# Kernel optimization log

Hardware: AMD Instinct MI355X
Metric: run time of the kernel (lower is better)

## Reference

```python
import jax, jax.numpy as jnp
import numpy as np

N = 50000          # nodes
E = 800000         # edges (avg degree 16)
FEATS = [96, 96, 96, 48]


def setup_inputs() -> dict:
    key = jax.random.key(0)
    ks = jax.random.split(key, 10)
    x = jax.random.normal(ks[0], (N, FEATS[0]), dtype=jnp.float32)
    edge_index = jax.random.randint(ks[1], (2, E), 0, N, dtype=jnp.int64)
    d = {"x": x, "edge_index": edge_index}
    i = 2
    for l in range(3):
        s = 1.0 / np.sqrt(FEATS[l])
        d[f"Wl{l}"] = jax.random.uniform(ks[i], (FEATS[l], FEATS[l + 1]), jnp.float32, -s, s); i += 1
        d[f"Wr{l}"] = jax.random.uniform(ks[i], (FEATS[l], FEATS[l + 1]), jnp.float32, -s, s); i += 1
        d[f"b{l}"] = jnp.zeros((FEATS[l + 1],), jnp.float32)
    return d


def _sage_layer(h, src, dst, Wl, Wr, b, n):
    # PyG SAGEConv (aggr='mean', root_weight=True, normalize=False):
    # out_i = W_l @ mean_{j in N(i)} h_j + W_r @ h_i + b
    msg = h[src]                                                   # [E, F] gather
    ssum = jax.ops.segment_sum(msg, dst, num_segments=n)           # [N, F] scatter-add
    cnt = jax.ops.segment_sum(jnp.ones((src.shape[0], 1), h.dtype), dst, num_segments=n)
    mean = ssum / jnp.maximum(cnt, 1.0)
    return mean @ Wl + h @ Wr + b


def reference(x, edge_index, Wl0, Wr0, b0, Wl1, Wr1, b1, Wl2, Wr2, b2):
    src, dst = edge_index[0], edge_index[1]
    n = x.shape[0]
    # block = SAGEConv -> ReLU -> dropout(identity in eval)
    h = jax.nn.relu(_sage_layer(x, src, dst, Wl0, Wr0, b0, n))
    h = jax.nn.relu(_sage_layer(h, src, dst, Wl1, Wr1, b1, n))
    h = jax.nn.relu(_sage_layer(h, src, dst, Wl2, Wr2, b2, n))
    return h
```

## Files before the change

### kernel.cpp

```cpp
#include <hip/hip_runtime.h>


#define NNODES 50000
#define NROWS  50001
#define ZROW   50000
#define NEDGES 800000
#define CAP    64
#define LSTR   72
#define NBKT   512
#define BKSZ   98
#define NBKB   511
#define EBA    400
#define EPBA   2000
#define SEGC   20
#define CVT_N8 600000
#define CB 2344
#define WTN 46080
#define WB 180

typedef __attribute__((ext_vector_type(8))) short bf16x8;
typedef __attribute__((ext_vector_type(4))) float f32x4;

__device__ inline unsigned short f2bf(float f) {
    unsigned int u = __float_as_uint(f);
    unsigned int r = (u + 0x7fffu + ((u >> 16) & 1u)) >> 16;
    return (unsigned short)r;
}
__device__ inline float bf2f_lo(unsigned int u) { return __uint_as_float(u << 16); }
__device__ inline float bf2f_hi(unsigned int u) { return __uint_as_float(u & 0xffff0000u); }

__global__ void build_a(const int* __restrict__ src, const int* __restrict__ dst,
                        unsigned int* __restrict__ region, unsigned char* __restrict__ cnta,
                        const float* __restrict__ x, unsigned short* __restrict__ h0b,
                        const float* __restrict__ Wl0, const float* __restrict__ Wr0,
                        const float* __restrict__ Wl1, const float* __restrict__ Wr1,
                        const float* __restrict__ Wl2, const float* __restrict__ Wr2,
                        unsigned short* __restrict__ WT0, unsigned short* __restrict__ WT1,
                        unsigned short* __restrict__ WT2) {
    int b = blockIdx.x;
    if (b < EBA) {
        __shared__ int hist[NBKT];
        const int t = threadIdx.x;
        for (int k = t; k < NBKT; k += 256) hist[k] = 0;
        __syncthreads();
        const int e0 = b * EPBA;
        for (int i = t; i < EPBA; i += 256) {
            int d = dst[e0 + i];
            int s = src[e0 + i];
            unsigned int bk = (unsigned int)d / 98u;
            unsigned int rel = (unsigned int)d - bk * 98u;
            unsigned int val = (rel << 16) | (unsigned int)s;
            int r = atomicAdd(&hist[bk], 1);
            if (r < SEGC) region[((size_t)b * NBKT + bk) * SEGC + r] = val;
        }
        __syncthreads();
        for (int k = t; k < NBKT; k += 256)
            cnta[(size_t)k * EBA + b] = (unsigned char)min(hist[k], SEGC);
    } else if (b < EBA + CB) {
        long long t = (long long)(b - EBA) * 256 + threadIdx.x;
        if (t < CVT_N8) {
            const float4* p = reinterpret_cast<const float4*>(x + t * 8);
            float4 a = p[0], c = p[1];
            uint4 o;
            o.x = (unsigned)f2bf(a.x) | ((unsigned)f2bf(a.y) << 16);
            o.y = (unsigned)f2bf(a.z) | ((unsigned)f2bf(a.w) << 16);
            o.z = (unsigned)f2bf(c.x) | ((unsigned)f2bf(c.y) << 16);
            o.w = (unsigned)f2bf(c.z) | ((unsigned)f2bf(c.w) << 16);
            *reinterpret_cast<uint4*>(h0b + t * 8) = o;
        }
    } else if (b < EBA + CB + WB) {
        int t = (b - EBA - CB) * 256 + threadIdx.x;
        if (t >= WTN) return;
        const float* Wl; const float* Wr; unsigned short* WT; int fout; int u;
        if (t < 18432)      { Wl = Wl0; Wr = Wr0; WT = WT0; fout = 96; u = t; }
        else if (t < 36864) { Wl = Wl1; Wr = Wr1; WT = WT1; fout = 96; u = t - 18432; }
        else                { Wl = Wl2; Wr = Wr2; WT = WT2; fout = 48; u = t - 36864; }
        int j = u / 192;
        int k = u - j * 192;
        float v = (k < 96) ? Wl[k * fout + j] : Wr[(k - 96) * fout + j];
        WT[u] = f2bf(v);
    } else {
        int t = threadIdx.x;
        if (t < 12) {
            uint4 z = make_uint4(0, 0, 0, 0);
            *reinterpret_cast<uint4*>(h0b + (size_t)ZROW * 96 + t * 8) = z;
        }
    }
}

__global__ __launch_bounds__(256) void build_b(const unsigned int* __restrict__ region,
                                               const unsigned char* __restrict__ cnta,
                                               int* __restrict__ deg,
                                               unsigned short* __restrict__ colu) {
    __shared__ unsigned char cnt_l[EBA];
    __shared__ int deg_l[BKSZ];
    __shared__ __attribute__((aligned(16))) unsigned short colu_l[BKSZ * CAP];
    const int k = blockIdx.x;
    const int t = threadIdx.x;
    const int base_node = k * BKSZ;
    const int nn = min(BKSZ, NNODES - base_node);
    for (int i = t; i < EBA; i += 256) cnt_l[i] = cnta[(size_t)k * EBA + i];
    if (t < BKSZ) deg_l[t] = 0;
    __syncthreads();

    for (int cb = t; cb < EBA; cb += 256) {
        const int c = cnt_l[cb];
        const unsigned int* cell = region + ((size_t)cb * NBKT + k) * SEGC;
        for (int j = 0; j < c; j += 4) {
            uint4 q = *reinterpret_cast<const uint4*>(cell + j);
            unsigned int qq0 = q.x, qq1 = q.y, qq2 = q.z, qq3 = q.w;
            if (j + 0 < c) {
                int local = (int)(qq0 >> 16);
                int r = atomicAdd(&deg_l[local], 1);
                if (r < CAP) colu_l[local * CAP + r] = (unsigned short)(qq0 & 0xffffu);
            }
            if (j + 1 < c) {
                int local = (int)(qq1 >> 16);
                int r = atomicAdd(&deg_l[local], 1);
                if (r < CAP) colu_l[local * CAP + r] = (unsigned short)(qq1 & 0xffffu);
            }
            if (j + 2 < c) {
                int local = (int)(qq2 >> 16);
                int r = atomicAdd(&deg_l[local], 1);
                if (r < CAP) colu_l[local * CAP + r] = (unsigned short)(qq2 & 0xffffu);
            }
            if (j + 3 < c) {
                int local = (int)(qq3 >> 16);
                int r = atomicAdd(&deg_l[local], 1);
                if (r < CAP) colu_l[local * CAP + r] = (unsigned short)(qq3 & 0xffffu);
            }
        }
    }
    __syncthreads();

    for (int i = t; i < nn * (CAP / 8); i += 256) {
        *reinterpret_cast<uint4*>(colu + (size_t)base_node * CAP + i * 8) =
            *reinterpret_cast<const uint4*>(colu_l + i * 8);
    }
    if (t < nn) deg[base_node + t] = deg_l[t];
}

template <int NT, bool WRITE_BF16>
__global__ __launch_bounds__(256) void fused_layer(
    const unsigned short* __restrict__ hb,
    const int* __restrict__ deg, const unsigned short* __restrict__ colu,
    const unsigned short* __restrict__ WT,
    const float* __restrict__ bias,
    unsigned short* __restrict__ out_bf, float* __restrict__ out_f) {
    __shared__ unsigned short Asm[16][200];
    __shared__ unsigned short cols[16 * LSTR];
    const int i0 = blockIdx.x * 16;
    const int t = threadIdx.x;

    if (WRITE_BF16 && blockIdx.x == 0 && t < 12) {
        uint4 z = make_uint4(0, 0, 0, 0);
        *reinterpret_cast<uint4*>(out_bf + (size_t)ZROW * 96 + t * 8) = z;
    }

    {
        int u4 = t * 4;
        int node = u4 >> 6;
        int slot = u4 & 63;
        uint2 v = *reinterpret_cast<const uint2*>(colu + (size_t)(i0 + node) * CAP + slot);
        int d = deg[i0 + node];
        unsigned int s0 = (slot + 0 < d) ? (v.x & 0xffffu) : ZROW;
        unsigned int s1 = (slot + 1 < d) ? (v.x >> 16)     : ZROW;
        unsigned int s2 = (slot + 2 < d) ? (v.y & 0xffffu) : ZROW;
        unsigned int s3 = (slot + 3 < d) ? (v.y >> 16)     : ZROW;
        uint2 o;
        o.x = s0 | (s1 << 16);
        o.y = s2 | (s3 << 16);
        *reinterpret_cast<uint2*>(&cols[node * LSTR + slot]) = o;
    }
    __syncthreads();

    if (t < 192) {
        const int nl = t / 12;
        const int c = (t - nl * 12) * 8;
        const int d = deg[i0 + nl];
        const int pd = (d + 7) & ~7;
        float a0 = 0.f, a1 = 0.f, a2 = 0.f, a3 = 0.f, a4 = 0.f, a5 = 0.f, a6 = 0.f, a7 = 0.f;
        for (int j = 0; j < pd; j += 8) {
            uint4 cu = *reinterpret_cast<const uint4*>(&cols[nl * LSTR + j]);
            int s0 = (int)(cu.x & 0xffffu), s1 = (int)(cu.x >> 16);
            int s2 = (int)(cu.y & 0xffffu), s3 = (int)(cu.y >> 16);
            int s4 = (int)(cu.z & 0xffffu), s5 = (int)(cu.z >> 16);
            int s6 = (int)(cu.w & 0xffffu), s7 = (int)(cu.w >> 16);
            uint4 u0 = *reinterpret_cast<const uint4*>(hb + (size_t)s0 * 96 + c);
            uint4 u1 = *reinterpret_cast<const uint4*>(hb + (size_t)s1 * 96 + c);
            uint4 u2 = *reinterpret_cast<const uint4*>(hb + (size_t)s2 * 96 + c);
            uint4 u3 = *reinterpret_cast<const uint4*>(hb + (size_t)s3 * 96 + c);
            uint4 u4 = *reinterpret_cast<const uint4*>(hb + (size_t)s4 * 96 + c);
            uint4 u5 = *reinterpret_cast<const uint4*>(hb + (size_t)s5 * 96 + c);
            uint4 u6 = *reinterpret_cast<const uint4*>(hb + (size_t)s6 * 96 + c);
            uint4 u7 = *reinterpret_cast<const uint4*>(hb + (size_t)s7 * 96 + c);
            a0 += bf2f_lo(u0.x) + bf2f_lo(u1.x) + bf2f_lo(u2.x) + bf2f_lo(u3.x)
                + bf2f_lo(u4.x) + bf2f_lo(u5.x) + bf2f_lo(u6.x) + bf2f_lo(u7.x);
            a1 += bf2f_hi(u0.x) + bf2f_hi(u1.x) + bf2f_hi(u2.x) + bf2f_hi(u3.x)
                + bf2f_hi(u4.x) + bf2f_hi(u5.x) + bf2f_hi(u6.x) + bf2f_hi(u7.x);
            a2 += bf2f_lo(u0.y) + bf2f_lo(u1.y) + bf2f_lo(u2.y) + bf2f_lo(u3.y)
                + bf2f_lo(u4.y) + bf2f_lo(u5.y) + bf2f_lo(u6.y) + bf2f_lo(u7.y);
            a3 += bf2f_hi(u0.y) + bf2f_hi(u1.y) + bf2f_hi(u2.y) + bf2f_hi(u3.y)
                + bf2f_hi(u4.y) + bf2f_hi(u5.y) + bf2f_hi(u6.y) + bf2f_hi(u7.y);
            a4 += bf2f_lo(u0.z) + bf2f_lo(u1.z) + bf2f_lo(u2.z) + bf2f_lo(u3.z)
                + bf2f_lo(u4.z) + bf2f_lo(u5.z) + bf2f_lo(u6.z) + bf2f_lo(u7.z);
            a5 += bf2f_hi(u0.z) + bf2f_hi(u1.z) + bf2f_hi(u2.z) + bf2f_hi(u3.z)
                + bf2f_hi(u4.z) + bf2f_hi(u5.z) + bf2f_hi(u6.z) + bf2f_hi(u7.z);
            a6 += bf2f_lo(u0.w) + bf2f_lo(u1.w) + bf2f_lo(u2.w) + bf2f_lo(u3.w)
                + bf2f_lo(u4.w) + bf2f_lo(u5.w) + bf2f_lo(u6.w) + bf2f_lo(u7.w);
            a7 += bf2f_hi(u0.w) + bf2f_hi(u1.w) + bf2f_hi(u2.w) + bf2f_hi(u3.w)
                + bf2f_hi(u4.w) + bf2f_hi(u5.w) + bf2f_hi(u6.w) + bf2f_hi(u7.w);
        }
        float inv = (d > 0) ? 1.0f / (float)d : 0.0f;
        uint4 o;
        o.x = (unsigned)f2bf(a0 * inv) | ((unsigned)f2bf(a1 * inv) << 16);
        o.y = (unsigned)f2bf(a2 * inv) | ((unsigned)f2bf(a3 * inv) << 16);
        o.z = (unsigned)f2bf(a4 * inv) | ((unsigned)f2bf(a5 * inv) << 16);
        o.w = (unsigned)f2bf(a6 * inv) | ((unsigned)f2bf(a7 * inv) << 16);
        *reinterpret_cast<uint4*>(&Asm[nl][c]) = o;
    }
    __syncthreads();

    const int wave = t >> 6;
    const int lane = t & 63;
    const int m = lane & 15;
    const int kq = (lane >> 4) * 8;

    bf16x8 afr[6];
#pragma unroll
    for (int kk = 0; kk < 3; ++kk)
        afr[kk] = *reinterpret_cast<const bf16x8*>(&Asm[m][kq + kk * 32]);
    const unsigned short* hrow = hb + (size_t)(i0 + m) * 96 + kq;
#pragma unroll
    for (int kk = 0; kk < 3; ++kk)
        afr[3 + kk] = *reinterpret_cast<const bf16x8*>(hrow + kk * 32);

    const int r0 = (lane >> 4) * 4;
    for (int nt = wave; nt < NT; nt += 4) {
        f32x4 acc = {0.f, 0.f, 0.f, 0.f};
        const unsigned short* wrow = WT + (size_t)(nt * 16 + m) * 192 + kq;
#pragma unroll
        for (int kk = 0; kk < 6; ++kk) {
            bf16x8 bfr = *reinterpret_cast<const bf16x8*>(wrow + kk * 32);
            acc = __builtin_amdgcn_mfma_f32_16x16x32_bf16(afr[kk], bfr, acc, 0, 0, 0);
        }
        int colj = nt * 16 + m;
        float bv = bias[colj];
#pragma unroll
        for (int r = 0; r < 4; ++r) {
            float v = fmaxf(acc[r] + bv, 0.0f);
            size_t oi = (size_t)(i0 + r0 + r) * (16 * NT) + colj;
            if (WRITE_BF16) out_bf[oi] = f2bf(v);
            else            out_f[oi] = v;
        }
    }
}

extern "C" void kernel_launch(void* const* d_in, const int* in_sizes, int n_in,
                              void* d_out, int out_size, void* d_ws, size_t ws_size,
                              hipStream_t stream) {
    const float* x   = (const float*)d_in[0];
    const int*   ei  = (const int*)d_in[1];
    const float* Wl0 = (const float*)d_in[2];
    const float* Wr0 = (const float*)d_in[3];
    const float* b0  = (const float*)d_in[4];
    const float* Wl1 = (const float*)d_in[5];
    const float* Wr1 = (const float*)d_in[6];
    const float* b1  = (const float*)d_in[7];
    const float* Wl2 = (const float*)d_in[8];
    const float* Wr2 = (const float*)d_in[9];
    const float* b2  = (const float*)d_in[10];
    float* out = (float*)d_out;

    const int* src = ei;
    const int* dst = ei + NEDGES;

    char* p = (char*)d_ws;
    int* deg = (int*)p;                        p += (size_t)50176 * 4;
    unsigned short* colu = (unsigned short*)p; p += (size_t)50176 * CAP * 2;
    unsigned char* cnta = (unsigned char*)p;   p += (size_t)NBKT * EBA;
    unsigned short* WT0 = (unsigned short*)p;  p += 96 * 192 * 2;
    unsigned short* WT1 = (unsigned short*)p;  p += 96 * 192 * 2;
    unsigned short* WT2 = (unsigned short*)p;  p += 48 * 192 * 2;
    unsigned short* h0b = (unsigned short*)p;  p += (size_t)NROWS * 96 * 2 + 64;
    unsigned short* h1b = (unsigned short*)p;  p += (size_t)NROWS * 96 * 2 + 64;
    unsigned short* h2b = (unsigned short*)p;  p += (size_t)NROWS * 96 * 2 + 64;

    unsigned int* region = (unsigned int*)h1b;

    build_a<<<EBA + CB + WB + 1, 256, 0, stream>>>(
        src, dst, region, cnta, x, h0b,
        Wl0, Wr0, Wl1, Wr1, Wl2, Wr2, WT0, WT1, WT2);

    build_b<<<NBKB, 256, 0, stream>>>(region, cnta, deg, colu);

    const int LB = NNODES / 16;
    fused_layer<6, true><<<LB, 256, 0, stream>>>(h0b, deg, colu, WT0, b0, h1b, nullptr);
    fused_layer<6, true><<<LB, 256, 0, stream>>>(h1b, deg, colu, WT1, b1, h2b, nullptr);
    fused_layer<3, false><<<LB, 256, 0, stream>>>(h2b, deg, colu, WT2, b2, nullptr, out);
}
```

Baseline: 200.4 us.

## Split bf16 features into 32-column planes and gather each plane separately

Stores node features as three 32-column bf16 planes, each holding 64 bytes per node, so every neighbor-gather pass touches a smaller working set that may fit in L2/LLC. Aggregation moves out of the fused layer into separate per-plane gather kernels that write the mean into a workspace buffer, followed by a standalone MFMA GEMM kernel. The trade is more kernel launches (four per layer), an extra round trip of the mean through global memory, and three reads of the CSR columns per layer, in exchange for better cache locality of the random gathers.

```diff
diff --git a/kernel.cpp b/kernel.cpp
--- a/kernel.cpp
+++ b/kernel.cpp
@@ -2,8 +2,8 @@
 
 
 #define NNODES 50000
-#define NROWS  50001
 #define ZROW   50000
+#define PST    1600512
 #define NEDGES 800000
 #define CAP    64
 #define LSTR   72
@@ -13,6 +13,7 @@
 #define EBA    400
 #define EPBA   2000
 #define SEGC   20
+#define SGB    782
 #define CVT_N8 600000
 #define CB 2344
 #define WTN 46080
@@ -59,14 +60,17 @@
     } else if (b < EBA + CB) {
         long long t = (long long)(b - EBA) * 256 + threadIdx.x;
         if (t < CVT_N8) {
-            const float4* p = reinterpret_cast<const float4*>(x + t * 8);
-            float4 a = p[0], c = p[1];
+            int row = (int)(t / 12);
+            int g = (int)(t - (long long)row * 12);
+            const float4* pp = reinterpret_cast<const float4*>(x + (size_t)row * 96 + g * 8);
+            float4 a = pp[0], c = pp[1];
             uint4 o;
             o.x = (unsigned)f2bf(a.x) | ((unsigned)f2bf(a.y) << 16);
             o.y = (unsigned)f2bf(a.z) | ((unsigned)f2bf(a.w) << 16);
             o.z = (unsigned)f2bf(c.x) | ((unsigned)f2bf(c.y) << 16);
             o.w = (unsigned)f2bf(c.z) | ((unsigned)f2bf(c.w) << 16);
-            *reinterpret_cast<uint4*>(h0b + t * 8) = o;
+            *reinterpret_cast<uint4*>(h0b + (size_t)(g >> 2) * PST + (size_t)row * 32
+                                      + (g & 3) * 8) = o;
         }
     } else if (b < EBA + CB + WB) {
         int t = (b - EBA - CB) * 256 + threadIdx.x;
@@ -83,7 +87,8 @@
         int t = threadIdx.x;
         if (t < 12) {
             uint4 z = make_uint4(0, 0, 0, 0);
-            *reinterpret_cast<uint4*>(h0b + (size_t)ZROW * 96 + t * 8) = z;
+            *reinterpret_cast<uint4*>(h0b + (size_t)(t >> 2) * PST + (size_t)ZROW * 32
+                                      + (t & 3) * 8) = z;
         }
     }
 }
@@ -140,29 +145,23 @@
     if (t < nn) deg[base_node + t] = deg_l[t];
 }
 
-template <int NT, bool WRITE_BF16>
-__global__ __launch_bounds__(256) void fused_layer(
+__global__ __launch_bounds__(256) void gather_slice(
     const unsigned short* __restrict__ hb,
     const int* __restrict__ deg, const unsigned short* __restrict__ colu,
-    const unsigned short* __restrict__ WT,
-    const float* __restrict__ bias,
-    unsigned short* __restrict__ out_bf, float* __restrict__ out_f) {
-    __shared__ unsigned short Asm[16][200];
-    __shared__ unsigned short cols[16 * LSTR];
-    const int i0 = blockIdx.x * 16;
+    unsigned short* __restrict__ Mb, int p) {
+    __shared__ unsigned short cols[64 * LSTR];
+    const int i0 = blockIdx.x * 64;
     const int t = threadIdx.x;
-
-    if (WRITE_BF16 && blockIdx.x == 0 && t < 12) {
-        uint4 z = make_uint4(0, 0, 0, 0);
-        *reinterpret_cast<uint4*>(out_bf + (size_t)ZROW * 96 + t * 8) = z;
-    }
-
-    {
-        int u4 = t * 4;
+    const int nn = min(64, NNODES - i0);
+
+#pragma unroll
+    for (int q = 0; q < 4; ++q) {
+        int item = t + q * 256;
+        int u4 = item * 4;
         int node = u4 >> 6;
         int slot = u4 & 63;
         uint2 v = *reinterpret_cast<const uint2*>(colu + (size_t)(i0 + node) * CAP + slot);
-        int d = deg[i0 + node];
+        int d = (node < nn) ? deg[i0 + node] : 0;
         unsigned int s0 = (slot + 0 < d) ? (v.x & 0xffffu) : ZROW;
         unsigned int s1 = (slot + 1 < d) ? (v.x >> 16)     : ZROW;
         unsigned int s2 = (slot + 2 < d) ? (v.y & 0xffffu) : ZROW;
@@ -174,52 +173,67 @@
     }
     __syncthreads();
 
-    if (t < 192) {
-        const int nl = t / 12;
-        const int c = (t - nl * 12) * 8;
-        const int d = deg[i0 + nl];
-        const int pd = (d + 7) & ~7;
-        float a0 = 0.f, a1 = 0.f, a2 = 0.f, a3 = 0.f, a4 = 0.f, a5 = 0.f, a6 = 0.f, a7 = 0.f;
-        for (int j = 0; j < pd; j += 8) {
-            uint4 cu = *reinterpret_cast<const uint4*>(&cols[nl * LSTR + j]);
-            int s0 = (int)(cu.x & 0xffffu), s1 = (int)(cu.x >> 16);
-            int s2 = (int)(cu.y & 0xffffu), s3 = (int)(cu.y >> 16);
-            int s4 = (int)(cu.z & 0xffffu), s5 = (int)(cu.z >> 16);
-            int s6 = (int)(cu.w & 0xffffu), s7 = (int)(cu.w >> 16);
-            uint4 u0 = *reinterpret_cast<const uint4*>(hb + (size_t)s0 * 96 + c);
-            uint4 u1 = *reinterpret_cast<const uint4*>(hb + (size_t)s1 * 96 + c);
-            uint4 u2 = *reinterpret_cast<const uint4*>(hb + (size_t)s2 * 96 + c);
-            uint4 u3 = *reinterpret_cast<const uint4*>(hb + (size_t)s3 * 96 + c);
-            uint4 u4 = *reinterpret_cast<const uint4*>(hb + (size_t)s4 * 96 + c);
-            uint4 u5 = *reinterpret_cast<const uint4*>(hb + (size_t)s5 * 96 + c);
-            uint4 u6 = *reinterpret_cast<const uint4*>(hb + (size_t)s6 * 96 + c);
-            uint4 u7 = *reinterpret_cast<const uint4*>(hb + (size_t)s7 * 96 + c);
-            a0 += bf2f_lo(u0.x) + bf2f_lo(u1.x) + bf2f_lo(u2.x) + bf2f_lo(u3.x)
-                + bf2f_lo(u4.x) + bf2f_lo(u5.x) + bf2f_lo(u6.x) + bf2f_lo(u7.x);
-            a1 += bf2f_hi(u0.x) + bf2f_hi(u1.x) + bf2f_hi(u2.x) + bf2f_hi(u3.x)
-                + bf2f_hi(u4.x) + bf2f_hi(u5.x) + bf2f_hi(u6.x) + bf2f_hi(u7.x);
-            a2 += bf2f_lo(u0.y) + bf2f_lo(u1.y) + bf2f_lo(u2.y) + bf2f_lo(u3.y)
-                + bf2f_lo(u4.y) + bf2f_lo(u5.y) + bf2f_lo(u6.y) + bf2f_lo(u7.y);
-            a3 += bf2f_hi(u0.y) + bf2f_hi(u1.y) + bf2f_hi(u2.y) + bf2f_hi(u3.y)
-                + bf2f_hi(u4.y) + bf2f_hi(u5.y) + bf2f_hi(u6.y) + bf2f_hi(u7.y);
-            a4 += bf2f_lo(u0.z) + bf2f_lo(u1.z) + bf2f_lo(u2.z) + bf2f_lo(u3.z)
-                + bf2f_lo(u4.z) + bf2f_lo(u5.z) + bf2f_lo(u6.z) + bf2f_lo(u7.z);
-            a5 += bf2f_hi(u0.z) + bf2f_hi(u1.z) + bf2f_hi(u2.z) + bf2f_hi(u3.z)
-                + bf2f_hi(u4.z) + bf2f_hi(u5.z) + bf2f_hi(u6.z) + bf2f_hi(u7.z);
-            a6 += bf2f_lo(u0.w) + bf2f_lo(u1.w) + bf2f_lo(u2.w) + bf2f_lo(u3.w)
-                + bf2f_lo(u4.w) + bf2f_lo(u5.w) + bf2f_lo(u6.w) + bf2f_lo(u7.w);
-            a7 += bf2f_hi(u0.w) + bf2f_hi(u1.w) + bf2f_hi(u2.w) + bf2f_hi(u3.w)
-                + bf2f_hi(u4.w) + bf2f_hi(u5.w) + bf2f_hi(u6.w) + bf2f_hi(u7.w);
-        }
-        float inv = (d > 0) ? 1.0f / (float)d : 0.0f;
-        uint4 o;
-        o.x = (unsigned)f2bf(a0 * inv) | ((unsigned)f2bf(a1 * inv) << 16);
-        o.y = (unsigned)f2bf(a2 * inv) | ((unsigned)f2bf(a3 * inv) << 16);
-        o.z = (unsigned)f2bf(a4 * inv) | ((unsigned)f2bf(a5 * inv) << 16);
-        o.w = (unsigned)f2bf(a6 * inv) | ((unsigned)f2bf(a7 * inv) << 16);
-        *reinterpret_cast<uint4*>(&Asm[nl][c]) = o;
-    }
-    __syncthreads();
+    const int nl = t >> 2;
+    const int cg = t & 3;
+    const unsigned short* hp = hb + (size_t)p * PST + cg * 8;
+    const int d = (nl < nn) ? deg[i0 + nl] : 0;
+    const int pd = (d + 7) & ~7;
+    float a0 = 0.f, a1 = 0.f, a2 = 0.f, a3 = 0.f, a4 = 0.f, a5 = 0.f, a6 = 0.f, a7 = 0.f;
+    for (int j = 0; j < pd; j += 8) {
+        uint4 cu = *reinterpret_cast<const uint4*>(&cols[nl * LSTR + j]);
+        int s0 = (int)(cu.x & 0xffffu), s1 = (int)(cu.x >> 16);
+        int s2 = (int)(cu.y & 0xffffu), s3 = (int)(cu.y >> 16);
+        int s4 = (int)(cu.z & 0xffffu), s5 = (int)(cu.z >> 16);
+        int s6 = (int)(cu.w & 0xffffu), s7 = (int)(cu.w >> 16);
+        uint4 u0 = *reinterpret_cast<const uint4*>(hp + (size_t)s0 * 32);
+        uint4 u1 = *reinterpret_cast<const uint4*>(hp + (size_t)s1 * 32);
+        uint4 u2 = *reinterpret_cast<const uint4*>(hp + (size_t)s2 * 32);
+        uint4 u3 = *reinterpret_cast<const uint4*>(hp + (size_t)s3 * 32);
+        uint4 u4 = *reinterpret_cast<const uint4*>(hp + (size_t)s4 * 32);
+        uint4 u5 = *reinterpret_cast<const uint4*>(hp + (size_t)s5 * 32);
+        uint4 u6 = *reinterpret_cast<const uint4*>(hp + (size_t)s6 * 32);
+        uint4 u7 = *reinterpret_cast<const uint4*>(hp + (size_t)s7 * 32);
+        a0 += bf2f_lo(u0.x) + bf2f_lo(u1.x) + bf2f_lo(u2.x) + bf2f_lo(u3.x)
+            + bf2f_lo(u4.x) + bf2f_lo(u5.x) + bf2f_lo(u6.x) + bf2f_lo(u7.x);
+        a1 += bf2f_hi(u0.x) + bf2f_hi(u1.x) + bf2f_hi(u2.x) + bf2f_hi(u3.x)
+            + bf2f_hi(u4.x) + bf2f_hi(u5.x) + bf2f_hi(u6.x) + bf2f_hi(u7.x);
+        a2 += bf2f_lo(u0.y) + bf2f_lo(u1.y) + bf2f_lo(u2.y) + bf2f_lo(u3.y)
+            + bf2f_lo(u4.y) + bf2f_lo(u5.y) + bf2f_lo(u6.y) + bf2f_lo(u7.y);
+        a3 += bf2f_hi(u0.y) + bf2f_hi(u1.y) + bf2f_hi(u2.y) + bf2f_hi(u3.y)
+            + bf2f_hi(u4.y) + bf2f_hi(u5.y) + bf2f_hi(u6.y) + bf2f_hi(u7.y);
+        a4 += bf2f_lo(u0.z) + bf2f_lo(u1.z) + bf2f_lo(u2.z) + bf2f_lo(u3.z)
+            + bf2f_lo(u4.z) + bf2f_lo(u5.z) + bf2f_lo(u6.z) + bf2f_lo(u7.z);
+        a5 += bf2f_hi(u0.z) + bf2f_hi(u1.z) + bf2f_hi(u2.z) + bf2f_hi(u3.z)
+            + bf2f_hi(u4.z) + bf2f_hi(u5.z) + bf2f_hi(u6.z) + bf2f_hi(u7.z);
+        a6 += bf2f_lo(u0.w) + bf2f_lo(u1.w) + bf2f_lo(u2.w) + bf2f_lo(u3.w)
+            + bf2f_lo(u4.w) + bf2f_lo(u5.w) + bf2f_lo(u6.w) + bf2f_lo(u7.w);
+        a7 += bf2f_hi(u0.w) + bf2f_hi(u1.w) + bf2f_hi(u2.w) + bf2f_hi(u3.w)
+            + bf2f_hi(u4.w) + bf2f_hi(u5.w) + bf2f_hi(u6.w) + bf2f_hi(u7.w);
+    }
+    float inv = (d > 0) ? 1.0f / (float)d : 0.0f;
+    uint4 o;
+    o.x = (unsigned)f2bf(a0 * inv) | ((unsigned)f2bf(a1 * inv) << 16);
+    o.y = (unsigned)f2bf(a2 * inv) | ((unsigned)f2bf(a3 * inv) << 16);
+    o.z = (unsigned)f2bf(a4 * inv) | ((unsigned)f2bf(a5 * inv) << 16);
+    o.w = (unsigned)f2bf(a6 * inv) | ((unsigned)f2bf(a7 * inv) << 16);
+    if (nl < nn)
+        *reinterpret_cast<uint4*>(Mb + (size_t)p * PST + (size_t)(i0 + nl) * 32 + cg * 8) = o;
+}
+
+template <int NT, bool WRITE_BF16>
+__global__ __launch_bounds__(256) void fused_gemm(
+    const unsigned short* __restrict__ Mb, const unsigned short* __restrict__ hb,
+    const unsigned short* __restrict__ WT,
+    const float* __restrict__ bias,
+    unsigned short* __restrict__ out_bf, float* __restrict__ out_f) {
+    const int i0 = blockIdx.x * 16;
+    const int t = threadIdx.x;
+
+    if (WRITE_BF16 && blockIdx.x == 0 && t < 12) {
+        uint4 z = make_uint4(0, 0, 0, 0);
+        *reinterpret_cast<uint4*>(out_bf + (size_t)(t >> 2) * PST + (size_t)ZROW * 32
+                                  + (t & 3) * 8) = z;
+    }
 
     const int wave = t >> 6;
     const int lane = t & 63;
@@ -229,11 +243,12 @@
     bf16x8 afr[6];
 #pragma unroll
     for (int kk = 0; kk < 3; ++kk)
-        afr[kk] = *reinterpret_cast<const bf16x8*>(&Asm[m][kq + kk * 32]);
-    const unsigned short* hrow = hb + (size_t)(i0 + m) * 96 + kq;
+        afr[kk] = *reinterpret_cast<const bf16x8*>(Mb + (size_t)kk * PST
+                                                   + (size_t)(i0 + m) * 32 + kq);
 #pragma unroll
     for (int kk = 0; kk < 3; ++kk)
-        afr[3 + kk] = *reinterpret_cast<const bf16x8*>(hrow + kk * 32);
+        afr[3 + kk] = *reinterpret_cast<const bf16x8*>(hb + (size_t)kk * PST
+                                                       + (size_t)(i0 + m) * 32 + kq);
 
     const int r0 = (lane >> 4) * 4;
     for (int nt = wave; nt < NT; nt += 4) {
@@ -249,9 +264,11 @@
 #pragma unroll
         for (int r = 0; r < 4; ++r) {
             float v = fmaxf(acc[r] + bv, 0.0f);
-            size_t oi = (size_t)(i0 + r0 + r) * (16 * NT) + colj;
-            if (WRITE_BF16) out_bf[oi] = f2bf(v);
-            else            out_f[oi] = v;
+            int row = i0 + r0 + r;
+            if (WRITE_BF16)
+                out_bf[(size_t)(colj >> 5) * PST + (size_t)row * 32 + (colj & 31)] = f2bf(v);
+            else
+                out_f[(size_t)row * 48 + colj] = v;
         }
     }
 }
@@ -282,9 +299,10 @@
     unsigned short* WT0 = (unsigned short*)p;  p += 96 * 192 * 2;
     unsigned short* WT1 = (unsigned short*)p;  p += 96 * 192 * 2;
     unsigned short* WT2 = (unsigned short*)p;  p += 48 * 192 * 2;
-    unsigned short* h0b = (unsigned short*)p;  p += (size_t)NROWS * 96 * 2 + 64;
-    unsigned short* h1b = (unsigned short*)p;  p += (size_t)NROWS * 96 * 2 + 64;
-    unsigned short* h2b = (unsigned short*)p;  p += (size_t)NROWS * 96 * 2 + 64;
+    unsigned short* h0b = (unsigned short*)p;  p += (size_t)3 * PST * 2 + 64;
+    unsigned short* h1b = (unsigned short*)p;  p += (size_t)3 * PST * 2 + 64;
+    unsigned short* h2b = (unsigned short*)p;  p += (size_t)3 * PST * 2 + 64;
+    unsigned short* Mb  = (unsigned short*)p;  p += (size_t)3 * PST * 2 + 64;
 
     unsigned int* region = (unsigned int*)h1b;
 
@@ -294,8 +312,20 @@
 
     build_b<<<NBKB, 256, 0, stream>>>(region, cnta, deg, colu);
 
-    const int LB = NNODES / 16;
-    fused_layer<6, true><<<LB, 256, 0, stream>>>(h0b, deg, colu, WT0, b0, h1b, nullptr);
-    fused_layer<6, true><<<LB, 256, 0, stream>>>(h1b, deg, colu, WT1, b1, h2b, nullptr);
-    fused_layer<3, false><<<LB, 256, 0, stream>>>(h2b, deg, colu, WT2, b2, nullptr, out);
-}
+    const int GB = NNODES / 16;
+
+    gather_slice<<<SGB, 256, 0, stream>>>(h0b, deg, colu, Mb, 0);
+    gather_slice<<<SGB, 256, 0, stream>>>(h0b, deg, colu, Mb, 1);
+    gather_slice<<<SGB, 256, 0, stream>>>(h0b, deg, colu, Mb, 2);
+    fused_gemm<6, true><<<GB, 256, 0, stream>>>(Mb, h0b, WT0, b0, h1b, nullptr);
+
+    gather_slice<<<SGB, 256, 0, stream>>>(h1b, deg, colu, Mb, 0);
+    gather_slice<<<SGB, 256, 0, stream>>>(h1b, deg, colu, Mb, 1);
+    gather_slice<<<SGB, 256, 0, stream>>>(h1b, deg, colu, Mb, 2);
+    fused_gemm<6, true><<<GB, 256, 0, stream>>>(Mb, h1b, WT1, b1, h2b, nullptr);
+
+    gather_slice<<<SGB, 256, 0, stream>>>(h2b, deg, colu, Mb, 0);
+    gather_slice<<<SGB, 256, 0, stream>>>(h2b, deg, colu, Mb, 1);
+    gather_slice<<<SGB, 256, 0, stream>>>(h2b, deg, colu, Mb, 2);
+    fused_gemm<3, false><<<GB, 256, 0, stream>>>(Mb, h2b, WT2, b2, nullptr, out);
+}
```

Result: slower. 254.5 us (+27.0%).
